# Performance work log

Measured on AMD Instinct MI355X. Metric: run time of the kernel, lower is better.

Reference implementation:

```python
import jax, jax.numpy as jnp
import numpy as np

N = 40000          # nodes
E = 640000         # edges (avg degree 16)
F_IN = 128         # num_node_features
H = 64             # hidden_channels
C_OUT = 32         # num_classes


def _glorot(key, fan_in, fan_out):
    lim = np.sqrt(6.0 / (fan_in + fan_out)).astype(np.float32)
    return jax.random.uniform(key, (fan_in, fan_out), jnp.float32, -lim, lim)


def setup_inputs() -> dict:
    key = jax.random.key(0)
    ks = jax.random.split(key, 12)
    x = jax.random.normal(ks[0], (N, F_IN), jnp.float32)
    edge_index = jax.random.randint(ks[1], (2, E), 0, N, dtype=jnp.int32)
    batch = jnp.zeros((N,), jnp.int32)  # unused by forward, kept for signature fidelity
    return {
        "x": x,
        "edge_index": edge_index,
        "batch": batch,
        "W1": _glorot(ks[2], F_IN, H),      "b1": jnp.zeros((H,), jnp.float32),
        "W2": _glorot(ks[3], H, 2 * H),     "b2": jnp.zeros((2 * H,), jnp.float32),
        "W3": _glorot(ks[4], 2 * H, 2 * H), "b3": jnp.zeros((2 * H,), jnp.float32),
        "W4": _glorot(ks[5], 2 * H, H),     "b4": jnp.zeros((H,), jnp.float32),
        "Wl": _glorot(ks[6], H, C_OUT),     "bl": jnp.zeros((C_OUT,), jnp.float32),
    }


def _gcn_norm(edge_index, n_nodes):
    """Add self-loops and compute symmetric D^{-1/2} A D^{-1/2} edge weights."""
    loop = jnp.arange(n_nodes, dtype=edge_index.dtype)
    src = jnp.concatenate([edge_index[0], loop])
    dst = jnp.concatenate([edge_index[1], loop])
    deg = jax.ops.segment_sum(jnp.ones_like(dst, dtype=jnp.float32), dst,
                              num_segments=n_nodes)
    d_inv_sqrt = jnp.where(deg > 0, jax.lax.rsqrt(deg), 0.0)
    norm = d_inv_sqrt[src] * d_inv_sqrt[dst]  # [E + N]
    return src, dst, norm


def _gcn_conv(h, W, b, src, dst, norm, n_nodes):
    h = h @ W                                   # [N, d_out] linear transform first
    msg = h[src] * norm[:, None]                # gather + edge scaling
    agg = jax.ops.segment_sum(msg, dst, num_segments=n_nodes)  # scatter-add
    return agg + b


def reference(x, edge_index, batch, W1, b1, W2, b2, W3, b3, W4, b4, Wl, bl):
    n_nodes = x.shape[0]
    src, dst, norm = _gcn_norm(edge_index, n_nodes)
    # eval mode: F.dropout(training=False) is identity
    h = jax.nn.relu(_gcn_conv(x, W1, b1, src, dst, norm, n_nodes))
    h = jax.nn.relu(_gcn_conv(h, W2, b2, src, dst, norm, n_nodes))
    h = jax.nn.relu(_gcn_conv(h, W3, b3, src, dst, norm, n_nodes))
    h = jax.nn.relu(_gcn_conv(h, W4, b4, src, dst, norm, n_nodes))
    return h @ Wl + bl  # [N, C_OUT]
```

## Files before the change

kernel.cpp:

```cpp
#include <hip/hip_runtime.h>
#include <hip/hip_bf16.h>


using bf16x8 = __attribute__((ext_vector_type(8))) __bf16;
using f32x4  = __attribute__((ext_vector_type(4))) float;

#define BUKCAP 8192

__device__ __forceinline__ int block_detect_bf16(const unsigned short* __restrict__ x16) {
    __shared__ int cnt;
    if (threadIdx.x == 0) cnt = 0;
    __syncthreads();
    if (threadIdx.x < 128) {
        unsigned e = (x16[2 * threadIdx.x] >> 7) & 0xFF;
        if (e >= 100 && e <= 135) atomicAdd(&cnt, 1);
    }
    __syncthreads();
    return cnt >= 64;
}

struct PrepDesc { const void* src; void* dst; int n; int mode; int dol2; int strideK; };
struct PrepArgs { PrepDesc d[12]; int pre[13]; int ndesc; };

__global__ __launch_bounds__(256) void prep_stage(PrepArgs a,
                                                  const unsigned short* __restrict__ x16,
                                                  int* __restrict__ flagG,
                                                  const int* __restrict__ src,
                                                  const int* __restrict__ dst,
                                                  int E, int NBUK,
                                                  int* __restrict__ bukFill,
                                                  unsigned* __restrict__ staging) {
    const int b = blockIdx.x;
    const int npre = a.pre[a.ndesc];
    if (b >= npre) {
        __shared__ int hist[160], start[160], run[160];
        const int t = threadIdx.x;
        const int base = (b - npre) * 4096;
        int sv[16], dv[16];
        #pragma unroll
        for (int j = 0; j < 16; ++j) {
            int e = base + j * 256 + t;
            if (e < E) { sv[j] = src[e]; dv[j] = dst[e]; } else dv[j] = -1;
        }
        if (t < NBUK) { hist[t] = 0; run[t] = 0; }
        __syncthreads();
        #pragma unroll
        for (int j = 0; j < 16; ++j)
            if (dv[j] >= 0) atomicAdd(&hist[dv[j] >> 8], 1);
        __syncthreads();
        if (t < NBUK && hist[t] > 0)
            start[t] = atomicAdd(&bukFill[t], hist[t]);
        __syncthreads();
        #pragma unroll
        for (int j = 0; j < 16; ++j) {
            if (dv[j] >= 0) {
                int bk = dv[j] >> 8;
                int slot = start[bk] + atomicAdd(&run[bk], 1);
                staging[(size_t)bk * BUKCAP + slot] = ((unsigned)dv[j] << 16) | (unsigned)sv[j];
            }
        }
        return;
    }
    const int fl = block_detect_bf16(x16);
    if (b == 0 && threadIdx.x == 0) *flagG = fl;
    int s = 0;
    for (; s < a.ndesc - 1; ++s) if (b < a.pre[s + 1]) break;
    const PrepDesc d = a.d[s];
    int i = (b - a.pre[s]) * 256 + threadIdx.x;
    if (i >= d.n) return;
    float v = fl ? __bfloat162float(((const __hip_bfloat16*)d.src)[i])
                 : ((const float*)d.src)[i];
    if (d.mode == 0) {
        ((float*)d.dst)[i] = v;
    } else {
        int k = i >> d.dol2;
        int col = i & ((1 << d.dol2) - 1);
        ((__hip_bfloat16*)d.dst)[col * d.strideK + k] = __float2bfloat16(v);
    }
}

template<int NTPW, bool RAW_A>
__device__ __forceinline__ void gemm_core(const void* __restrict__ Ain,
                                          const __hip_bfloat16* __restrict__ WT,
                                          __hip_bfloat16* __restrict__ out,
                                          int d_in, int d_out_log2, int strideK,
                                          bool bfmode, int blk, int tid) {
    const int wave = tid >> 6, lane = tid & 63;
    const int m = lane & 15, quad = lane >> 4;
    const int rowBase = blk * 64;
    const int nkc = d_in >> 5;
    const int nt0 = wave * NTPW;

    f32x4 acc[4][NTPW];
    #pragma unroll
    for (int rt = 0; rt < 4; ++rt)
        #pragma unroll
        for (int j = 0; j < NTPW; ++j)
            acc[rt][j] = (f32x4){0.f, 0.f, 0.f, 0.f};

    auto mainloop = [&](bool asBF) {
        for (int kc = 0; kc < nkc; ++kc) {
            const int koff = (kc << 5) + quad * 8;
            bf16x8 a[4];
            #pragma unroll
            for (int rt = 0; rt < 4; ++rt) {
                const size_t off = (size_t)(rowBase + rt * 16 + m) * d_in + koff;
                if (!RAW_A || asBF) {
                    a[rt] = *(const bf16x8*)((const __hip_bfloat16*)Ain + off);
                } else {
                    const float* p = (const float*)Ain + off;
                    float4 f0 = *(const float4*)p;
                    float4 f1 = *(const float4*)(p + 4);
                    union { bf16x8 v; __hip_bfloat16 h[8]; } u;
                    u.h[0] = __float2bfloat16(f0.x); u.h[1] = __float2bfloat16(f0.y);
                    u.h[2] = __float2bfloat16(f0.z); u.h[3] = __float2bfloat16(f0.w);
                    u.h[4] = __float2bfloat16(f1.x); u.h[5] = __float2bfloat16(f1.y);
                    u.h[6] = __float2bfloat16(f1.z); u.h[7] = __float2bfloat16(f1.w);
                    a[rt] = u.v;
                }
            }
            #pragma unroll
            for (int j = 0; j < NTPW; ++j) {
                const int n = ((nt0 + j) << 4) + m;
                bf16x8 b = *(const bf16x8*)&WT[n * strideK + koff];
                #pragma unroll
                for (int rt = 0; rt < 4; ++rt)
                    acc[rt][j] = __builtin_amdgcn_mfma_f32_16x16x32_bf16(a[rt], b, acc[rt][j], 0, 0, 0);
            }
        }
    };
    if (bfmode) mainloop(true); else mainloop(false);

    const int d_out = 1 << d_out_log2;
    #pragma unroll
    for (int rt = 0; rt < 4; ++rt) {
        const int row = rowBase + rt * 16 + quad * 4;
        #pragma unroll
        for (int j = 0; j < NTPW; ++j) {
            const int col = ((nt0 + j) << 4) + m;
            #pragma unroll
            for (int r = 0; r < 4; ++r)
                out[(size_t)(row + r) * d_out + col] = __float2bfloat16(acc[rt][j][r]);
        }
    }
}

__global__ __launch_bounds__(256) void hist_gemm(const unsigned* __restrict__ staging,
                                                 const int* __restrict__ bukFill,
                                                 float* __restrict__ dinv,
                                                 int2* __restrict__ rowSE,
                                                 int N, int NBUK,
                                                 const void* __restrict__ x,
                                                 const __hip_bfloat16* __restrict__ WT0,
                                                 __hip_bfloat16* __restrict__ lin1,
                                                 int strideK0,
                                                 const int* __restrict__ flag) {
    if ((int)blockIdx.x < NBUK) {
        __shared__ int hist[256];
        __shared__ int pfx[256];
        const int t = threadIdx.x;
        hist[t] = 0;
        __syncthreads();
        const int fill = bukFill[blockIdx.x];
        const unsigned* st = staging + (size_t)blockIdx.x * BUKCAP;
        for (int k = t; k < fill; k += 256)
            atomicAdd(&hist[(st[k] >> 16) & 255], 1);
        __syncthreads();
        const int c = hist[t];
        const int cp = (c + 7) & ~7;
        pfx[t] = cp;
        __syncthreads();
        for (int off = 1; off < 256; off <<= 1) {
            int v = (t >= off) ? pfx[t - off] : 0;
            __syncthreads();
            pfx[t] += v;
            __syncthreads();
        }
        const int i = (blockIdx.x << 8) + t;
        if (i < N) {
            const int start = blockIdx.x * BUKCAP + pfx[t] - cp;
            rowSE[i] = make_int2(start, start + cp);
            dinv[i] = rsqrtf((float)(c + 1));
        }
        return;
    }
    gemm_core<1, true>(x, WT0, lin1, 128, 6, strideK0,
                       (*flag != 0), blockIdx.x - NBUK, threadIdx.x);
}

__global__ __launch_bounds__(256) void scatter_csr(const unsigned* __restrict__ staging,
                                                   const int* __restrict__ bukFill,
                                                   const float* __restrict__ dinv,
                                                   const int2* __restrict__ rowSE,
                                                   unsigned* __restrict__ csr32,
                                                   int N) {
    __shared__ int cur[256];
    const int t = threadIdx.x;
    const int i = (blockIdx.x << 8) + t;
    int2 se = (i < N) ? rowSE[i] : make_int2(0, 0);
    cur[t] = se.x;
    __syncthreads();
    const int fill = bukFill[blockIdx.x];
    const unsigned* st = staging + (size_t)blockIdx.x * BUKCAP;
    for (int k = t; k < fill; k += 256) {
        unsigned u = st[k];
        int s = (int)(u & 0xffffu);
        int loc = (u >> 16) & 255;
        int pos = atomicAdd(&cur[loc], 1);
        union { __hip_bfloat16 h; unsigned short w16; } cv;
        cv.h = __float2bfloat16(dinv[s]);
        csr32[pos] = ((unsigned)cv.w16 << 16) | (unsigned)s;
    }
    __syncthreads();
    for (int p = cur[t]; p < se.y; ++p) csr32[p] = 0u;
}

template<int W>
__device__ __forceinline__ void gather_acc8w(const __hip_bfloat16* __restrict__ Hin,
                                             int cb, int node, float di,
                                             const int2* __restrict__ rowSE,
                                             const unsigned* __restrict__ csr32,
                                             float acc[8]) {
    const __hip_bfloat16* base = Hin + cb;
    auto loadrow = [&](unsigned u) -> uint4 {
        return *(const uint4*)(base + (size_t)(u & 0xffffu) * W);
    };
    auto wof = [](unsigned u) -> float {
        return __int_as_float((int)(u & 0xffff0000u));
    };
    auto accumw = [&](uint4 v, float w) {
        union { uint4 q; __hip_bfloat162 h2[4]; } c;
        c.q = v;
        #pragma unroll
        for (int j = 0; j < 4; ++j) {
            float2 p = __bfloat1622float2(c.h2[j]);
            acc[2 * j]     += w * p.x;
            acc[2 * j + 1] += w * p.y;
        }
    };
    #pragma unroll
    for (int j = 0; j < 8; ++j) acc[j] = 0.f;
    accumw(*(const uint4*)(base + (size_t)node * W), di);
    const int2 se = rowSE[node];
    int e = se.x;
    const int e1 = se.y;
    for (; e + 16 <= e1; e += 16) {
        uint4 i0 = *(const uint4*)(csr32 + e);
        uint4 i1 = *(const uint4*)(csr32 + e + 4);
        uint4 i2 = *(const uint4*)(csr32 + e + 8);
        uint4 i3 = *(const uint4*)(csr32 + e + 12);
        uint4 r0 = loadrow(i0.x), r1 = loadrow(i0.y), r2 = loadrow(i0.z), r3 = loadrow(i0.w);
        uint4 r4 = loadrow(i1.x), r5 = loadrow(i1.y), r6 = loadrow(i1.z), r7 = loadrow(i1.w);
        uint4 r8 = loadrow(i2.x), r9 = loadrow(i2.y), ra = loadrow(i2.z), rb = loadrow(i2.w);
        uint4 rc = loadrow(i3.x), rd = loadrow(i3.y), re = loadrow(i3.z), rf = loadrow(i3.w);
        accumw(r0, wof(i0.x)); accumw(r1, wof(i0.y)); accumw(r2, wof(i0.z)); accumw(r3, wof(i0.w));
        accumw(r4, wof(i1.x)); accumw(r5, wof(i1.y)); accumw(r6, wof(i1.z)); accumw(r7, wof(i1.w));
        accumw(r8, wof(i2.x)); accumw(r9, wof(i2.y)); accumw(ra, wof(i2.z)); accumw(rb, wof(i2.w));
        accumw(rc, wof(i3.x)); accumw(rd, wof(i3.y)); accumw(re, wof(i3.z)); accumw(rf, wof(i3.w));
    }
    if (e < e1) {
        uint4 i0 = *(const uint4*)(csr32 + e);
        uint4 i1 = *(const uint4*)(csr32 + e + 4);
        uint4 r0 = loadrow(i0.x), r1 = loadrow(i0.y), r2 = loadrow(i0.z), r3 = loadrow(i0.w);
        uint4 r4 = loadrow(i1.x), r5 = loadrow(i1.y), r6 = loadrow(i1.z), r7 = loadrow(i1.w);
        accumw(r0, wof(i0.x)); accumw(r1, wof(i0.y)); accumw(r2, wof(i0.z)); accumw(r3, wof(i0.w));
        accumw(r4, wof(i1.x)); accumw(r5, wof(i1.y)); accumw(r6, wof(i1.z)); accumw(r7, wof(i1.w));
    }
}

__global__ __launch_bounds__(256) void gather8(const __hip_bfloat16* __restrict__ Hin,
                                               const int2* __restrict__ rowSE,
                                               const unsigned* __restrict__ csr32,
                                               const float* __restrict__ dinv,
                                               const float* __restrict__ b,
                                               __hip_bfloat16* __restrict__ out, int n) {
    const int t = blockIdx.x * 256 + threadIdx.x;
    const int node = t >> 3;
    const int f = t & 7;
    if (node >= n) return;
    const int cb = f * 8;
    const float di = dinv[node];
    float acc[8];
    gather_acc8w<64>(Hin, cb, node, di, rowSE, csr32, acc);
    union { uint4 v; __hip_bfloat16 h[8]; } p;
    #pragma unroll
    for (int j = 0; j < 8; ++j)
        p.h[j] = __float2bfloat16(fmaxf(di * acc[j] + b[cb + j], 0.f));
    *(uint4*)(out + (size_t)node * 64 + cb) = p.v;
}

template<int D_IN, int NTPW>
__global__ __launch_bounds__(256) void gather_gemm(const __hip_bfloat16* __restrict__ Hin,
                                                   const int2* __restrict__ rowSE,
                                                   const unsigned* __restrict__ csr32,
                                                   const float* __restrict__ dinv,
                                                   const __hip_bfloat16* __restrict__ WT,
                                                   const float* __restrict__ bias,
                                                   __hip_bfloat16* __restrict__ out,
                                                   int d_out_log2) {
    constexpr int SK = D_IN + 8;
    __shared__ __align__(16) __hip_bfloat16 sG[64 * SK];
    const int tid = threadIdx.x;
    const int rowBase = blockIdx.x * 64;
    constexpr int TPR = D_IN / 8;
    constexpr int NPP = 256 / TPR;
    #pragma unroll
    for (int pass = 0; pass < 64 / NPP; ++pass) {
        const int local = pass * NPP + tid / TPR;
        const int node = rowBase + local;
        const int cb = (tid % TPR) * 8;
        const float di = dinv[node];
        float acc[8];
        gather_acc8w<D_IN>(Hin, cb, node, di, rowSE, csr32, acc);
        union { bf16x8 v; __hip_bfloat16 h[8]; } p;
        #pragma unroll
        for (int j = 0; j < 8; ++j) p.h[j] = __float2bfloat16(di * acc[j]);
        *(bf16x8*)&sG[local * SK + cb] = p.v;
    }
    __syncthreads();

    const int wave = tid >> 6, lane = tid & 63;
    const int m = lane & 15, quad = lane >> 4;
    const int nkc = D_IN >> 5;
    const int nt0 = wave * NTPW;

    f32x4 acc2[4][NTPW];
    #pragma unroll
    for (int rt = 0; rt < 4; ++rt)
        #pragma unroll
        for (int j = 0; j < NTPW; ++j)
            acc2[rt][j] = (f32x4){0.f, 0.f, 0.f, 0.f};

    for (int kc = 0; kc < nkc; ++kc) {
        const int koff = (kc << 5) + quad * 8;
        bf16x8 a[4];
        #pragma unroll
        for (int rt = 0; rt < 4; ++rt)
            a[rt] = *(const bf16x8*)&sG[(rt * 16 + m) * SK + koff];
        #pragma unroll
        for (int j = 0; j < NTPW; ++j) {
            const int n = ((nt0 + j) << 4) + m;
            bf16x8 b = *(const bf16x8*)&WT[n * SK + koff];
            #pragma unroll
            for (int rt = 0; rt < 4; ++rt)
                acc2[rt][j] = __builtin_amdgcn_mfma_f32_16x16x32_bf16(a[rt], b, acc2[rt][j], 0, 0, 0);
        }
    }

    const int d_out = 1 << d_out_log2;
    #pragma unroll
    for (int rt = 0; rt < 4; ++rt) {
        const int row = rowBase + rt * 16 + quad * 4;
        #pragma unroll
        for (int j = 0; j < NTPW; ++j) {
            const int col = ((nt0 + j) << 4) + m;
            const float bv = bias[col];
            #pragma unroll
            for (int r = 0; r < 4; ++r)
                out[(size_t)(row + r) * d_out + col] =
                    __float2bfloat16(fmaxf(acc2[rt][j][r] + bv, 0.f));
        }
    }
}

__global__ __launch_bounds__(256) void gather_gemm34(const __hip_bfloat16* __restrict__ Hin,
                                                     const int2* __restrict__ rowSE,
                                                     const unsigned* __restrict__ csr32,
                                                     const float* __restrict__ dinv,
                                                     const __hip_bfloat16* __restrict__ WT3,
                                                     const float* __restrict__ b3,
                                                     const __hip_bfloat16* __restrict__ WT4,
                                                     __hip_bfloat16* __restrict__ lin4) {
    constexpr int SK = 136;
    __shared__ __align__(16) __hip_bfloat16 sG[64 * SK];
    const int tid = threadIdx.x;
    const int rowBase = blockIdx.x * 64;

    #pragma unroll
    for (int pass = 0; pass < 4; ++pass) {
        const int local = pass * 16 + tid / 16;
        const int node = rowBase + local;
        const int cb = (tid % 16) * 8;
        const float di = dinv[node];
        float acc[8];
        gather_acc8w<128>(Hin, cb, node, di, rowSE, csr32, acc);
        union { bf16x8 v; __hip_bfloat16 h[8]; } p;
        #pragma unroll
        for (int j = 0; j < 8; ++j) p.h[j] = __float2bfloat16(di * acc[j]);
        *(bf16x8*)&sG[local * SK + cb] = p.v;
    }
    __syncthreads();

    const int wave = tid >> 6, lane = tid & 63;
    const int m = lane & 15, quad = lane >> 4;

    f32x4 acc2[4][2];
    #pragma unroll
    for (int rt = 0; rt < 4; ++rt)
        #pragma unroll
        for (int j = 0; j < 2; ++j)
            acc2[rt][j] = (f32x4){0.f, 0.f, 0.f, 0.f};
    for (int kc = 0; kc < 4; ++kc) {
        const int koff = (kc << 5) + quad * 8;
        bf16x8 a[4];
        #pragma unroll
        for (int rt = 0; rt < 4; ++rt)
            a[rt] = *(const bf16x8*)&sG[(rt * 16 + m) * SK + koff];
        #pragma unroll
        for (int j = 0; j < 2; ++j) {
            const int n = ((wave * 2 + j) << 4) + m;
            bf16x8 b = *(const bf16x8*)&WT3[n * SK + koff];
            #pragma unroll
            for (int rt = 0; rt < 4; ++rt)
                acc2[rt][j] = __builtin_amdgcn_mfma_f32_16x16x32_bf16(a[rt], b, acc2[rt][j], 0, 0, 0);
        }
    }
    __syncthreads();

    #pragma unroll
    for (int j = 0; j < 2; ++j) {
        const int col = ((wave * 2 + j) << 4) + m;
        const float bv = b3[col];
        #pragma unroll
        for (int rt = 0; rt < 4; ++rt) {
            const int row = rt * 16 + quad * 4;
            #pragma unroll
            for (int r = 0; r < 4; ++r)
                sG[(row + r) * SK + col] = __float2bfloat16(fmaxf(acc2[rt][j][r] + bv, 0.f));
        }
    }
    __syncthreads();

    f32x4 acc3[4];
    #pragma unroll
    for (int rt = 0; rt < 4; ++rt) acc3[rt] = (f32x4){0.f, 0.f, 0.f, 0.f};
    for (int kc = 0; kc < 4; ++kc) {
        const int koff = (kc << 5) + quad * 8;
        bf16x8 a[4];
        #pragma unroll
        for (int rt = 0; rt < 4; ++rt)
            a[rt] = *(const bf16x8*)&sG[(rt * 16 + m) * SK + koff];
        const int n = (wave << 4) + m;
        bf16x8 b = *(const bf16x8*)&WT4[n * SK + koff];
        #pragma unroll
        for (int rt = 0; rt < 4; ++rt)
            acc3[rt] = __builtin_amdgcn_mfma_f32_16x16x32_bf16(a[rt], b, acc3[rt], 0, 0, 0);
    }
    const int col = (wave << 4) + m;
    #pragma unroll
    for (int rt = 0; rt < 4; ++rt) {
        const int row = rowBase + rt * 16 + quad * 4;
        #pragma unroll
        for (int r = 0; r < 4; ++r)
            lin4[(size_t)(row + r) * 64 + col] = __float2bfloat16(acc3[rt][r]);
    }
}

__global__ __launch_bounds__(256) void gather_final(const __hip_bfloat16* __restrict__ Hin,
                                                    const int2* __restrict__ rowSE,
                                                    const unsigned* __restrict__ csr32,
                                                    const float* __restrict__ dinv,
                                                    const float* __restrict__ b4,
                                                    const float* __restrict__ Wlf,
                                                    const float* __restrict__ blf,
                                                    void* __restrict__ out,
                                                    const int* __restrict__ flag) {
    __shared__ float sWl[64 * 32];
    __shared__ float sH[32 * 65];
    const int tid = threadIdx.x;
    for (int i = tid; i < 2048; i += 256) sWl[i] = Wlf[i];
    const int nl = tid >> 3, j = tid & 7, cb = j * 8;
    const int node = blockIdx.x * 32 + nl;
    const float di = dinv[node];
    float acc[8];
    gather_acc8w<64>(Hin, cb, node, di, rowSE, csr32, acc);
    #pragma unroll
    for (int k = 0; k < 8; ++k)
        sH[nl * 65 + cb + k] = fmaxf(di * acc[k] + b4[cb + k], 0.f);
    __syncthreads();
    float4 r = *(const float4*)(blf + 4 * j);
    for (int k = 0; k < 64; ++k) {
        const float hv = sH[nl * 65 + k];
        const float4 w = *(const float4*)&sWl[k * 32 + 4 * j];
        r.x += hv * w.x; r.y += hv * w.y; r.z += hv * w.z; r.w += hv * w.w;
    }
    const size_t idx = (size_t)node * 32 + 4 * j;
    if (*flag) {
        union { __hip_bfloat16 h[4]; uint2 u; } p;
        p.h[0] = __float2bfloat16(r.x); p.h[1] = __float2bfloat16(r.y);
        p.h[2] = __float2bfloat16(r.z); p.h[3] = __float2bfloat16(r.w);
        *(uint2*)((__hip_bfloat16*)out + idx) = p.u;
    } else {
        *(float4*)((float*)out + idx) = r;
    }
}

extern "C" void kernel_launch(void* const* d_in, const int* in_sizes, int n_in,
                              void* d_out, int out_size, void* d_ws, size_t ws_size,
                              hipStream_t stream) {
    const int* edge = (const int*)d_in[1];
    const int F_IN = 128;
    const int N = in_sizes[0] / F_IN;
    const int E = in_sizes[1] / 2;
    const int* src = edge;
    const int* dst = edge + E;
    const int NBUK = (N + 255) >> 8;

    auto align256 = [](size_t v) { return (v + 255) & ~(size_t)255; };
    char* ws = (char*)d_ws;
    int*   flag    = (int*)ws;    ws += 256;
    float* dinv    = (float*)ws;  ws += align256((size_t)N * 4);
    int2*  rowSE   = (int2*)ws;   ws += align256((size_t)N * 8);
    int*   bukFill = (int*)ws;    ws += align256((size_t)NBUK * 4);
    unsigned* csr32   = (unsigned*)ws; ws += align256((size_t)NBUK * BUKCAP * 4);
    unsigned* staging = (unsigned*)ws; ws += align256((size_t)NBUK * BUKCAP * 4);
    __hip_bfloat16* Hbuf = (__hip_bfloat16*)ws; ws += align256((size_t)N * 128 * 2);
    __hip_bfloat16* Tbuf = (__hip_bfloat16*)ws; ws += align256((size_t)N * 128 * 2);

    const int widx[4] = {3, 5, 7, 9};
    const int bidx[4] = {4, 6, 8, 10};
    float* Bc[4];
    for (int i = 0; i < 4; ++i) { Bc[i] = (float*)ws; ws += align256((size_t)in_sizes[bidx[i]] * 4); }
    float* Wlf = (float*)ws; ws += align256((size_t)in_sizes[11] * 4);
    float* blf = (float*)ws; ws += align256((size_t)in_sizes[12] * 4);

    const int LD_IN[4]  = {128, 64, 128, 128};
    const int LD_OL2[4] = {6, 7, 7, 6};
    int strideK[4];
    __hip_bfloat16* WT[4];
    for (int l = 0; l < 4; ++l) {
        strideK[l] = LD_IN[l] + 8;
        WT[l] = (__hip_bfloat16*)ws;
        ws += align256((size_t)(1 << LD_OL2[l]) * strideK[l] * 2);
    }

    hipMemsetAsync(bukFill, 0, (size_t)NBUK * 4, stream);

    PrepArgs pa{};
    int nd = 0, pre = 0;
    auto addDesc = [&](const void* s, void* d, int n, int mode, int dol2, int sk) {
        pa.d[nd] = {s, d, n, mode, dol2, sk};
        pa.pre[nd] = pre;
        pre += (n + 255) / 256;
        nd++;
    };
    for (int l = 0; l < 4; ++l)
        addDesc(d_in[widx[l]], WT[l], LD_IN[l] << LD_OL2[l], 1, LD_OL2[l], strideK[l]);
    for (int l = 0; l < 4; ++l)
        addDesc(d_in[bidx[l]], Bc[l], in_sizes[bidx[l]], 0, 0, 0);
    addDesc(d_in[11], Wlf, in_sizes[11], 0, 0, 0);
    addDesc(d_in[12], blf, in_sizes[12], 0, 0, 0);
    pa.pre[nd] = pre;
    pa.ndesc = nd;
    const int SB = (E + 4095) / 4096;
    prep_stage<<<pre + SB, 256, 0, stream>>>(pa, (const unsigned short*)d_in[0], flag,
                                             src, dst, E, NBUK, bukFill, staging);

    const int nblk = N / 64;
    const int g64  = (N * 8 + 255) / 256;

    hist_gemm<<<NBUK + nblk, 256, 0, stream>>>(staging, bukFill, dinv, rowSE, N, NBUK,
                                               d_in[0], WT[0], Tbuf, strideK[0], flag);

    scatter_csr<<<NBUK, 256, 0, stream>>>(staging, bukFill, dinv, rowSE, csr32, N);

    gather8<<<g64, 256, 0, stream>>>(Tbuf, rowSE, csr32, dinv, Bc[0], Hbuf, N);

    gather_gemm<64, 2><<<nblk, 256, 0, stream>>>(Hbuf, rowSE, csr32, dinv, WT[1], Bc[1], Tbuf, 7);

    gather_gemm34<<<nblk, 256, 0, stream>>>(Tbuf, rowSE, csr32, dinv, WT[2], Bc[2], WT[3], Hbuf);

    gather_final<<<g64, 256, 0, stream>>>(Hbuf, rowSE, csr32, dinv, Bc[3], Wlf, blf, d_out, flag);
}
```

Before: 195.8 us.

## Compute node degrees globally in prep and fuse CSR scatter into prefix kernel

Per-node in-degrees are now counted with global atomics during the bucketing pass, so the second kernel no longer needs a per-bucket histogram over staging before its prefix scan. With degrees known up front, the CSR scatter (which computes source dinv directly from the degree array) is folded into the same kernel, removing one launch and one re-read of staging. The cost is 640K extra global atomics in the prep stage and a larger memset. The scatter blocks also now share a kernel with the first-layer GEMM blocks.

```diff
diff --git a/kernel.cpp b/kernel.cpp
--- a/kernel.cpp
+++ b/kernel.cpp
@@ -29,6 +29,7 @@
                                                   const int* __restrict__ dst,
                                                   int E, int NBUK,
                                                   int* __restrict__ bukFill,
+                                                  int* __restrict__ degG,
                                                   unsigned* __restrict__ staging) {
     const int b = blockIdx.x;
     const int npre = a.pre[a.ndesc];
@@ -46,7 +47,10 @@
         __syncthreads();
         #pragma unroll
         for (int j = 0; j < 16; ++j)
-            if (dv[j] >= 0) atomicAdd(&hist[dv[j] >> 8], 1);
+            if (dv[j] >= 0) {
+                atomicAdd(&hist[dv[j] >> 8], 1);
+                atomicAdd(&degG[dv[j]], 1);
+            }
         __syncthreads();
         if (t < NBUK && hist[t] > 0)
             start[t] = atomicAdd(&bukFill[t], hist[t]);
@@ -145,28 +149,24 @@
     }
 }
 
-__global__ __launch_bounds__(256) void hist_gemm(const unsigned* __restrict__ staging,
-                                                 const int* __restrict__ bukFill,
-                                                 float* __restrict__ dinv,
-                                                 int2* __restrict__ rowSE,
-                                                 int N, int NBUK,
-                                                 const void* __restrict__ x,
-                                                 const __hip_bfloat16* __restrict__ WT0,
-                                                 __hip_bfloat16* __restrict__ lin1,
-                                                 int strideK0,
-                                                 const int* __restrict__ flag) {
+__global__ __launch_bounds__(256) void prefix_scatter_gemm(const unsigned* __restrict__ staging,
+                                                           const int* __restrict__ bukFill,
+                                                           const int* __restrict__ degG,
+                                                           float* __restrict__ dinv,
+                                                           int2* __restrict__ rowSE,
+                                                           unsigned* __restrict__ csr32,
+                                                           int N, int NBUK,
+                                                           const void* __restrict__ x,
+                                                           const __hip_bfloat16* __restrict__ WT0,
+                                                           __hip_bfloat16* __restrict__ lin1,
+                                                           int strideK0,
+                                                           const int* __restrict__ flag) {
     if ((int)blockIdx.x < NBUK) {
-        __shared__ int hist[256];
         __shared__ int pfx[256];
+        __shared__ int cur[256];
         const int t = threadIdx.x;
-        hist[t] = 0;
-        __syncthreads();
-        const int fill = bukFill[blockIdx.x];
-        const unsigned* st = staging + (size_t)blockIdx.x * BUKCAP;
-        for (int k = t; k < fill; k += 256)
-            atomicAdd(&hist[(st[k] >> 16) & 255], 1);
-        __syncthreads();
-        const int c = hist[t];
+        const int i = (blockIdx.x << 8) + t;
+        const int c = (i < N) ? degG[i] : 0;
         const int cp = (c + 7) & ~7;
         pfx[t] = cp;
         __syncthreads();
@@ -176,43 +176,31 @@
             pfx[t] += v;
             __syncthreads();
         }
-        const int i = (blockIdx.x << 8) + t;
+        const int start = blockIdx.x * BUKCAP + pfx[t] - cp;
         if (i < N) {
-            const int start = blockIdx.x * BUKCAP + pfx[t] - cp;
             rowSE[i] = make_int2(start, start + cp);
             dinv[i] = rsqrtf((float)(c + 1));
         }
+        cur[t] = start;
+        __syncthreads();
+        const int fill = bukFill[blockIdx.x];
+        const unsigned* st = staging + (size_t)blockIdx.x * BUKCAP;
+        for (int k = t; k < fill; k += 256) {
+            unsigned u = st[k];
+            int s = (int)(u & 0xffffu);
+            int loc = (u >> 16) & 255;
+            int pos = atomicAdd(&cur[loc], 1);
+            union { __hip_bfloat16 h; unsigned short w16; } cv;
+            cv.h = __float2bfloat16(rsqrtf((float)(degG[s] + 1)));
+            csr32[pos] = ((unsigned)cv.w16 << 16) | (unsigned)s;
+        }
+        __syncthreads();
+        const int e1 = start + cp;
+        for (int p = cur[t]; p < e1; ++p) csr32[p] = 0u;
         return;
     }
     gemm_core<1, true>(x, WT0, lin1, 128, 6, strideK0,
                        (*flag != 0), blockIdx.x - NBUK, threadIdx.x);
-}
-
-__global__ __launch_bounds__(256) void scatter_csr(const unsigned* __restrict__ staging,
-                                                   const int* __restrict__ bukFill,
-                                                   const float* __restrict__ dinv,
-                                                   const int2* __restrict__ rowSE,
-                                                   unsigned* __restrict__ csr32,
-                                                   int N) {
-    __shared__ int cur[256];
-    const int t = threadIdx.x;
-    const int i = (blockIdx.x << 8) + t;
-    int2 se = (i < N) ? rowSE[i] : make_int2(0, 0);
-    cur[t] = se.x;
-    __syncthreads();
-    const int fill = bukFill[blockIdx.x];
-    const unsigned* st = staging + (size_t)blockIdx.x * BUKCAP;
-    for (int k = t; k < fill; k += 256) {
-        unsigned u = st[k];
-        int s = (int)(u & 0xffffu);
-        int loc = (u >> 16) & 255;
-        int pos = atomicAdd(&cur[loc], 1);
-        union { __hip_bfloat16 h; unsigned short w16; } cv;
-        cv.h = __float2bfloat16(dinv[s]);
-        csr32[pos] = ((unsigned)cv.w16 << 16) | (unsigned)s;
-    }
-    __syncthreads();
-    for (int p = cur[t]; p < se.y; ++p) csr32[p] = 0u;
 }
 
 template<int W>
@@ -512,6 +500,7 @@
     float* dinv    = (float*)ws;  ws += align256((size_t)N * 4);
     int2*  rowSE   = (int2*)ws;   ws += align256((size_t)N * 8);
     int*   bukFill = (int*)ws;    ws += align256((size_t)NBUK * 4);
+    int*   degG    = (int*)ws;    ws += align256((size_t)N * 4);
     unsigned* csr32   = (unsigned*)ws; ws += align256((size_t)NBUK * BUKCAP * 4);
     unsigned* staging = (unsigned*)ws; ws += align256((size_t)NBUK * BUKCAP * 4);
     __hip_bfloat16* Hbuf = (__hip_bfloat16*)ws; ws += align256((size_t)N * 128 * 2);
@@ -534,7 +523,8 @@
         ws += align256((size_t)(1 << LD_OL2[l]) * strideK[l] * 2);
     }
 
-    hipMemsetAsync(bukFill, 0, (size_t)NBUK * 4, stream);
+    const size_t zlen = (size_t)((char*)degG + (size_t)N * 4 - (char*)bukFill);
+    hipMemsetAsync(bukFill, 0, zlen, stream);
 
     PrepArgs pa{};
     int nd = 0, pre = 0;
@@ -554,15 +544,14 @@
     pa.ndesc = nd;
     const int SB = (E + 4095) / 4096;
     prep_stage<<<pre + SB, 256, 0, stream>>>(pa, (const unsigned short*)d_in[0], flag,
-                                             src, dst, E, NBUK, bukFill, staging);
+                                             src, dst, E, NBUK, bukFill, degG, staging);
 
     const int nblk = N / 64;
     const int g64  = (N * 8 + 255) / 256;
 
-    hist_gemm<<<NBUK + nblk, 256, 0, stream>>>(staging, bukFill, dinv, rowSE, N, NBUK,
-                                               d_in[0], WT[0], Tbuf, strideK[0], flag);
-
-    scatter_csr<<<NBUK, 256, 0, stream>>>(staging, bukFill, dinv, rowSE, csr32, N);
+    prefix_scatter_gemm<<<NBUK + nblk, 256, 0, stream>>>(staging, bukFill, degG, dinv, rowSE,
+                                                         csr32, N, NBUK,
+                                                         d_in[0], WT[0], Tbuf, strideK[0], flag);
 
     gather8<<<g64, 256, 0, stream>>>(Tbuf, rowSE, csr32, dinv, Bc[0], Hbuf, N);
 
```

Result: slower. 217.7 us (+11.2%).
